# Optimization experiments

Measured on AMD Instinct MI355X. Metric: run time of the kernel, lower is better.

Reference implementation:

```python
import jax, jax.numpy as jnp
import numpy as np

N_NODES = 100000


def gcn_conv(x, W, b, src, dst, ew, n):
    """PyG GCNConv with edge_weight: add self-loops (weight 1), symmetric norm,
    linear transform, scatter-add aggregation, bias."""
    h = x @ W                                   # [N, F_out]
    # degree includes the self-loop weight of 1 per node
    deg = jnp.zeros((n,), dtype=x.dtype).at[dst].add(ew) + 1.0
    dinv = jax.lax.rsqrt(deg)                   # deg > 0 always (self-loop)
    norm = dinv[src] * ew * dinv[dst]           # [E]
    agg = jax.ops.segment_sum(h[src] * norm[:, None], dst, num_segments=n)
    # self-loop contribution: norm_ii = dinv[i]^2 * 1
    agg = agg + h * (dinv * dinv)[:, None]
    return agg + b


def setup_inputs() -> dict:
    key = jax.random.key(0)
    ks = jax.random.split(key, 9)
    N, E, F_in, F_h, F_out = N_NODES, 1600000, 128, 64, 10
    x = jax.random.normal(ks[0], (N, F_in), dtype=jnp.float32)
    edge_index = jax.random.randint(ks[1], (2, E), 0, N, dtype=jnp.int64)
    edge_weight = jax.random.uniform(ks[2], (E,), dtype=jnp.float32)
    def glorot(k, fi, fo):
        s = jnp.sqrt(6.0 / (fi + fo))
        return jax.random.uniform(k, (fi, fo), minval=-s, maxval=s, dtype=jnp.float32)
    return {
        "x": x,
        "edge_index": edge_index,
        "edge_weight": edge_weight,
        "W1": glorot(ks[3], F_in, F_h), "b1": jnp.zeros((F_h,), jnp.float32),
        "W2": glorot(ks[4], F_h, F_h), "b2": jnp.zeros((F_h,), jnp.float32),
        "Wfc": glorot(ks[5], F_h, F_out), "bfc": jnp.zeros((F_out,), jnp.float32),
    }


def reference(x, edge_index, edge_weight, W1, b1, W2, b2, Wfc, bfc):
    n = x.shape[0]
    src, dst = edge_index[0], edge_index[1]
    h = gcn_conv(x, W1, b1, src, dst, edge_weight, n)
    h = jax.nn.relu(h)
    h = gcn_conv(h, W2, b2, src, dst, edge_weight, n)
    h = jax.nn.relu(h)
    return h @ Wfc + bfc
```

## Files before the change

### kernel.cpp

```cpp
#include <hip/hip_runtime.h>

static constexpr int F_IN  = 128;
static constexpr int F_H   = 64;
static constexpr int F_OUT = 10;

static constexpr int NPB_SHIFT = 9;
static constexpr int NPB = 1 << NPB_SHIFT;
static constexpr int MAXC = 256;
static constexpr int EPB = 4096;

__device__ __forceinline__ unsigned short f2bf(float f) {
    unsigned u = __float_as_uint(f);
    return (unsigned short)((u + 0x7fff + ((u >> 16) & 1)) >> 16);
}
__device__ __forceinline__ float bf_lo(unsigned u) { return __uint_as_float(u << 16); }
__device__ __forceinline__ float bf_hi(unsigned u) { return __uint_as_float(u & 0xffff0000u); }

__device__ __forceinline__ int load_idx(const void* ein, bool f64, long i) {
    return f64 ? (int)((const long long*)ein)[i] : ((const int*)ein)[i];
}

__global__ __launch_bounds__(256) void k_detect_init(const unsigned long long* __restrict__ u,
                                                     int* __restrict__ flag,
                                                     int* __restrict__ gcur) {
    int tid = threadIdx.x;
    if (tid < MAXC) gcur[tid] = 0;
    if (tid < 64) {
        unsigned long long v = u[tid];
        int hz = ((v >> 32) == 0ull) ? 1 : 0;
        int all64 = __all(hz);
        if (tid == 0) flag[0] = all64;
    }
}

__global__ __launch_bounds__(256) void k_part1(const void* __restrict__ ein,
                                               const float* __restrict__ ew,
                                               const int* __restrict__ flag,
                                               int* __restrict__ gcur,
                                               unsigned long long* __restrict__ packed,
                                               int E, int NC, int cap) {
    __shared__ int lcnt[MAXC];
    __shared__ int lofs[MAXC];
    int tid = threadIdx.x;
    if (tid < NC) lcnt[tid] = 0;
    __syncthreads();
    bool f = flag[0];
    int base = blockIdx.x * EPB;
#pragma unroll
    for (int j = 0; j < EPB / 256; ++j) {
        int e = base + j * 256 + tid;
        if (e < E) {
            int d = load_idx(ein, f, (long)E + e);
            atomicAdd(&lcnt[d >> NPB_SHIFT], 1);
        }
    }
    __syncthreads();
    if (tid < NC) {
        int c = lcnt[tid];
        lofs[tid] = c ? atomicAdd(&gcur[tid], c) : 0;
        lcnt[tid] = 0;
    }
    __syncthreads();
#pragma unroll
    for (int j = 0; j < EPB / 256; ++j) {
        int e = base + j * 256 + tid;
        if (e < E) {
            int s = load_idx(ein, f, e);
            int d = load_idx(ein, f, (long)E + e);
            unsigned int wb = __float_as_uint(ew[e]);
            int b = d >> NPB_SHIFT;
            int pos = lofs[b] + atomicAdd(&lcnt[b], 1);
            if (pos < cap) {
                unsigned long long u = (unsigned long long)wb
                                     | ((unsigned long long)(unsigned)s << 32)
                                     | ((unsigned long long)(unsigned)(d & (NPB - 1)) << 49);
                packed[(long)b * cap + pos] = u;
            }
        }
    }
}

__global__ __launch_bounds__(256) void k_chist(const unsigned long long* __restrict__ packed,
                                               const int* __restrict__ gcur,
                                               int* __restrict__ rp,
                                               int* __restrict__ pbt,
                                               float* __restrict__ dinv,
                                               int N, int cap) {
    __shared__ int   lc[NPB];
    __shared__ float ld[NPB];
    __shared__ int   sm[256];
    int b = blockIdx.x, tid = threadIdx.x;
#pragma unroll
    for (int i = tid; i < NPB; i += 256) { lc[i] = 0; ld[i] = 0.0f; }
    __syncthreads();
    int cnt = gcur[b];
    const unsigned long long* pk = packed + (long)b * cap;
    for (int p = tid; p < cnt; p += 256) {
        unsigned long long u = pk[p];
        int dl = (int)(u >> 49);
        atomicAdd(&lc[dl], 1);
        atomicAdd(&ld[dl], __uint_as_float((unsigned int)u));
    }
    __syncthreads();
    int c0 = lc[tid * 2], c1 = lc[tid * 2 + 1];
    int pp0 = (c0 + 15) & ~15, pp1 = (c1 + 15) & ~15;
    int s = pp0 + pp1;
    sm[tid] = s;
    __syncthreads();
    for (int off = 1; off < 256; off <<= 1) {
        int v = 0;
        if (tid >= off) v = sm[tid - off];
        __syncthreads();
        sm[tid] += v;
        __syncthreads();
    }
    int excl = sm[tid] - s;
    int n0 = b << NPB_SHIFT;
    int node0 = n0 + tid * 2, node1 = node0 + 1;
    if (node0 < N) {
        rp[node0]   = excl;
        dinv[node0] = rsqrtf(ld[tid * 2] + 1.0f);
    }
    if (node1 < N) {
        rp[node1]   = excl + pp0;
        dinv[node1] = rsqrtf(ld[tid * 2 + 1] + 1.0f);
    }
    if (tid == 255) pbt[b] = sm[255];
}

__global__ __launch_bounds__(256) void k_scanP(const int* __restrict__ pbt,
                                               int* __restrict__ pbase,
                                               int* __restrict__ rp, int NC, int N) {
    __shared__ int sm[256];
    int tid = threadIdx.x;
    int c = (tid < NC) ? pbt[tid] : 0;
    sm[tid] = c;
    __syncthreads();
    for (int off = 1; off < 256; off <<= 1) {
        int v = 0;
        if (tid >= off) v = sm[tid - off];
        __syncthreads();
        sm[tid] += v;
        __syncthreads();
    }
    if (tid < NC) pbase[tid] = sm[tid] - c;
    if (tid == 255) rp[N] = sm[255];
}

__global__ __launch_bounds__(256) void k_rpfix(int* __restrict__ rp,
                                               const int* __restrict__ pbase, int N) {
    int i = blockIdx.x * 256 + threadIdx.x;
    if (i < N) rp[i] += pbase[i >> NPB_SHIFT];
}

__global__ __launch_bounds__(256) void k_cscatter(const unsigned long long* __restrict__ packed,
                                                  const int* __restrict__ gcur,
                                                  const int* __restrict__ rp,
                                                  const float* __restrict__ dinv,
                                                  uint2* __restrict__ recs,
                                                  int N, int cap) {
    __shared__ int   cur[NPB];
    __shared__ float dd[NPB];
    int b = blockIdx.x, tid = threadIdx.x;
    int n0 = b << NPB_SHIFT;
#pragma unroll
    for (int i = tid; i < NPB; i += 256) {
        int node = n0 + i;
        cur[i] = (node < N) ? rp[node]   : 0;
        dd[i]  = (node < N) ? dinv[node] : 0.0f;
    }
    __syncthreads();
    int cnt = gcur[b];
    const unsigned long long* pk = packed + (long)b * cap;
    for (int p = tid; p < cnt; p += 256) {
        unsigned long long u = pk[p];
        int dl = (int)(u >> 49);
        int s  = (int)((u >> 32) & 0x1FFFF);
        float w = __uint_as_float((unsigned int)u);
        int pos = atomicAdd(&cur[dl], 1);
        uint2 r;
        r.x = (unsigned)(s << 7);
        r.y = __float_as_uint(dinv[s] * w * dd[dl]);
        recs[pos] = r;
    }
    __syncthreads();
    for (int i = tid; i < NPB; i += 256) {
        int node = n0 + i;
        if (node < N) {
            int end = rp[node + 1];
            for (int p = cur[i]; p < end; ++p) recs[p] = make_uint2(0u, 0u);
        }
    }
}

template <int K>
__global__ __launch_bounds__(256) void k_gemm(const float* __restrict__ A,
                                              const float* __restrict__ W,
                                              unsigned short* __restrict__ Cb, int M) {
    __shared__ float As[128][32];
    __shared__ float Ws[32][64];
    int tid = threadIdx.x;
    int tx = tid & 15;
    int ty = tid >> 4;
    int rb = blockIdx.x * 128;
    float acc[8][4] = {};
    for (int kc = 0; kc < K; kc += 32) {
        __syncthreads();
#pragma unroll
        for (int i = 0; i < 4; ++i) {
            int e = tid + i * 256;
            int r = e >> 3, g = e & 7;
            int gr = rb + r;
            float4 v = make_float4(0.f, 0.f, 0.f, 0.f);
            if (gr < M) v = *(const float4*)&A[(long)gr * K + kc + g * 4];
            int gs = g ^ ((r >> 3) & 7);
            *(float4*)&As[r][gs * 4] = v;
        }
#pragma unroll
        for (int i = 0; i < 2; ++i) {
            int e = tid + i * 256;
            int k = e >> 4, n4 = e & 15;
            *(float4*)&Ws[k][n4 * 4] = *(const float4*)&W[(long)(kc + k) * 64 + n4 * 4];
        }
        __syncthreads();
#pragma unroll
        for (int g = 0; g < 8; ++g) {
            float4 b0 = *(const float4*)&Ws[g * 4 + 0][tx * 4];
            float4 b1 = *(const float4*)&Ws[g * 4 + 1][tx * 4];
            float4 b2 = *(const float4*)&Ws[g * 4 + 2][tx * 4];
            float4 b3 = *(const float4*)&Ws[g * 4 + 3][tx * 4];
            int gs = (g ^ (ty & 7)) * 4;
#pragma unroll
            for (int rr = 0; rr < 8; ++rr) {
                float4 a = *(const float4*)&As[ty * 8 + rr][gs];
                acc[rr][0] = fmaf(a.x, b0.x, acc[rr][0]);
                acc[rr][1] = fmaf(a.x, b0.y, acc[rr][1]);
                acc[rr][2] = fmaf(a.x, b0.z, acc[rr][2]);
                acc[rr][3] = fmaf(a.x, b0.w, acc[rr][3]);
                acc[rr][0] = fmaf(a.y, b1.x, acc[rr][0]);
                acc[rr][1] = fmaf(a.y, b1.y, acc[rr][1]);
                acc[rr][2] = fmaf(a.y, b1.z, acc[rr][2]);
                acc[rr][3] = fmaf(a.y, b1.w, acc[rr][3]);
                acc[rr][0] = fmaf(a.z, b2.x, acc[rr][0]);
                acc[rr][1] = fmaf(a.z, b2.y, acc[rr][1]);
                acc[rr][2] = fmaf(a.z, b2.z, acc[rr][2]);
                acc[rr][3] = fmaf(a.z, b2.w, acc[rr][3]);
                acc[rr][0] = fmaf(a.w, b3.x, acc[rr][0]);
                acc[rr][1] = fmaf(a.w, b3.y, acc[rr][1]);
                acc[rr][2] = fmaf(a.w, b3.z, acc[rr][2]);
                acc[rr][3] = fmaf(a.w, b3.w, acc[rr][3]);
            }
        }
    }
#pragma unroll
    for (int rr = 0; rr < 8; ++rr) {
        int gr = rb + ty * 8 + rr;
        if (gr < M) {
            ushort4 v;
            v.x = f2bf(acc[rr][0]); v.y = f2bf(acc[rr][1]);
            v.z = f2bf(acc[rr][2]); v.w = f2bf(acc[rr][3]);
            *(ushort4*)&Cb[(long)gr * 64 + tx * 4] = v;
        }
    }
}

__global__ __launch_bounds__(256, 4) void k_agg(const unsigned short* __restrict__ hb,
                                                const int* __restrict__ rp,
                                                const uint2* __restrict__ recs,
                                                const float* __restrict__ dinv,
                                                const float* __restrict__ bias,
                                                float* __restrict__ out, int N) {
    int wid  = (blockIdx.x * 256 + threadIdx.x) >> 6;
    int lane = threadIdx.x & 63;
    int fg   = lane & 15;
    int es   = lane >> 4;
    if (wid >= N) return;
    int fg8 = fg * 8;
    const char* hbase = (const char*)hb;
    int p0 = rp[wid], p1 = rp[wid + 1];
    float a0 = 0.f, a1 = 0.f, a2 = 0.f, a3 = 0.f;
    for (int pb = p0 + es * 4; pb < p1; pb += 16) {
        uint4 r01 = *(const uint4*)&recs[pb];
        uint4 r23 = *(const uint4*)&recs[pb + 2];
        uint2 h0 = *(const uint2*)(hbase + r01.x + fg8);
        uint2 h1 = *(const uint2*)(hbase + r01.z + fg8);
        uint2 h2 = *(const uint2*)(hbase + r23.x + fg8);
        uint2 h3 = *(const uint2*)(hbase + r23.z + fg8);
        float w0 = __uint_as_float(r01.y), w1 = __uint_as_float(r01.w);
        float w2 = __uint_as_float(r23.y), w3 = __uint_as_float(r23.w);
        a0 = fmaf(w0, bf_lo(h0.x), a0); a1 = fmaf(w0, bf_hi(h0.x), a1);
        a2 = fmaf(w0, bf_lo(h0.y), a2); a3 = fmaf(w0, bf_hi(h0.y), a3);
        a0 = fmaf(w1, bf_lo(h1.x), a0); a1 = fmaf(w1, bf_hi(h1.x), a1);
        a2 = fmaf(w1, bf_lo(h1.y), a2); a3 = fmaf(w1, bf_hi(h1.y), a3);
        a0 = fmaf(w2, bf_lo(h2.x), a0); a1 = fmaf(w2, bf_hi(h2.x), a1);
        a2 = fmaf(w2, bf_lo(h2.y), a2); a3 = fmaf(w2, bf_hi(h2.y), a3);
        a0 = fmaf(w3, bf_lo(h3.x), a0); a1 = fmaf(w3, bf_hi(h3.x), a1);
        a2 = fmaf(w3, bf_lo(h3.y), a2); a3 = fmaf(w3, bf_hi(h3.y), a3);
    }
#pragma unroll
    for (int m = 16; m <= 32; m <<= 1) {
        a0 += __shfl_xor(a0, m);
        a1 += __shfl_xor(a1, m);
        a2 += __shfl_xor(a2, m);
        a3 += __shfl_xor(a3, m);
    }
    float di  = dinv[wid];
    float di2 = di * di;
    uint2 hs = *(const uint2*)(hbase + ((long)wid << 7) + fg8);
    float4 bv = *(const float4*)&bias[fg * 4];
    a0 = fmaf(bf_lo(hs.x), di2, a0 + bv.x);
    a1 = fmaf(bf_hi(hs.x), di2, a1 + bv.y);
    a2 = fmaf(bf_lo(hs.y), di2, a2 + bv.z);
    a3 = fmaf(bf_hi(hs.y), di2, a3 + bv.w);
    if (es == 0) {
        float4 r = make_float4(fmaxf(a0, 0.f), fmaxf(a1, 0.f),
                               fmaxf(a2, 0.f), fmaxf(a3, 0.f));
        *(float4*)&out[(long)wid * 64 + fg * 4] = r;
    }
}

__global__ __launch_bounds__(256) void k_fc(const float* __restrict__ h,
                                            const float* __restrict__ W,
                                            const float* __restrict__ b,
                                            float* __restrict__ out, int N) {
    __shared__ float Ws[64 * 10];
    __shared__ float bs[16];
    int tid = threadIdx.x;
    for (int e = tid; e < 64 * 10; e += 256) Ws[e] = W[e];
    if (tid < 10) bs[tid] = b[tid];
    __syncthreads();
    int i = blockIdx.x * 256 + tid;
    if (i >= N) return;
    float acc[10];
#pragma unroll
    for (int j = 0; j < 10; ++j) acc[j] = bs[j];
    const float4* row = (const float4*)&h[(long)i * 64];
#pragma unroll
    for (int c = 0; c < 16; ++c) {
        float4 a = row[c];
#pragma unroll
        for (int j = 0; j < 10; ++j) {
            acc[j] = fmaf(a.x, Ws[(4 * c + 0) * 10 + j], acc[j]);
            acc[j] = fmaf(a.y, Ws[(4 * c + 1) * 10 + j], acc[j]);
            acc[j] = fmaf(a.z, Ws[(4 * c + 2) * 10 + j], acc[j]);
            acc[j] = fmaf(a.w, Ws[(4 * c + 3) * 10 + j], acc[j]);
        }
    }
#pragma unroll
    for (int j = 0; j < 10; ++j) out[(long)i * 10 + j] = acc[j];
}

extern "C" void kernel_launch(void* const* d_in, const int* in_sizes, int n_in,
                              void* d_out, int out_size, void* d_ws, size_t ws_size,
                              hipStream_t stream) {
    const float* x    = (const float*)d_in[0];
    const void*  eidx = d_in[1];
    const float* ew   = (const float*)d_in[2];
    const float* W1   = (const float*)d_in[3];
    const float* b1   = (const float*)d_in[4];
    const float* W2   = (const float*)d_in[5];
    const float* b2   = (const float*)d_in[6];
    const float* Wfc  = (const float*)d_in[7];
    const float* bfc  = (const float*)d_in[8];
    float* out = (float*)d_out;

    const int N  = in_sizes[0] / F_IN;
    const int E  = in_sizes[2];
    const int NC = (N + NPB - 1) >> NPB_SHIFT;
    const int cap = E / NC + E / (8 * NC) + 1024;

    char* w = (char*)d_ws;
    size_t off = 0;
    auto alloc = [&](size_t bytes) {
        void* p = w + off;
        off += (bytes + 255) & ~(size_t)255;
        return p;
    };
    float* dinv  = (float*)alloc((size_t)N * 4);
    int*   rp    = (int*)alloc((size_t)(N + 1) * 4);
    int*   flag  = (int*)alloc(256);
    int*   gcur  = (int*)alloc((size_t)MAXC * 4);
    int*   pbt   = (int*)alloc((size_t)MAXC * 4);
    int*   pbase = (int*)alloc((size_t)MAXC * 4);
    unsigned long long* packed =
        (unsigned long long*)alloc((size_t)NC * cap * 8);
    uint2* recs  = (uint2*)alloc(((size_t)E + 15u * (size_t)N + 64) * 8);
    unsigned short* h1b = (unsigned short*)alloc((size_t)N * F_H * 2);
    float* g1    = (float*)alloc((size_t)N * F_H * 4);
    unsigned short* h2b = h1b;
    float* g2    = g1;
    (void)ws_size;

    const int PB = (E + EPB - 1) / EPB;

    k_detect_init<<<1, 256, 0, stream>>>((const unsigned long long*)eidx, flag, gcur);
    k_part1<<<PB, 256, 0, stream>>>(eidx, ew, flag, gcur, packed, E, NC, cap);
    k_chist<<<NC, 256, 0, stream>>>(packed, gcur, rp, pbt, dinv, N, cap);
    k_scanP<<<1, 256, 0, stream>>>(pbt, pbase, rp, NC, N);
    k_rpfix<<<(N + 255) / 256, 256, 0, stream>>>(rp, pbase, N);
    k_cscatter<<<NC, 256, 0, stream>>>(packed, gcur, rp, dinv, recs, N, cap);

    const int GB = (N + 127) / 128;
    k_gemm<F_IN><<<GB, 256, 0, stream>>>(x, W1, h1b, N);
    k_agg<<<(N + 3) / 4, 256, 0, stream>>>(h1b, rp, recs, dinv, b1, g1, N);
    k_gemm<F_H><<<GB, 256, 0, stream>>>(g1, W2, h2b, N);
    k_agg<<<(N + 3) / 4, 256, 0, stream>>>(h2b, rp, recs, dinv, b2, g2, N);
    k_fc<<<(N + 255) / 256, 256, 0, stream>>>(g2, Wfc, bfc, out, N);
}
```

Measured before the change: 215.9 us.

## Store aggregation outputs as bf16 and fold rowptr fixup into scatter kernel

The aggregation kernels now write their ReLU'd outputs as bf16 instead of fp32, and the second GEMM and the final FC read bf16 inputs. This halves the bytes of the intermediate feature buffers. The k_detect_init and k_rpfix launches are removed: the index-width flag is computed per block inside k_part1, gcur is cleared with a memset, and absolute row pointers are built inside k_cscatter from the per-partition base. Rounding the layer outputs to bf16 adds some precision loss, and an extra rowptr array is written.

New measurement: 216.9 us. No clear change (+0.5%).

```diff
diff --git a/kernel.cpp b/kernel.cpp
--- a/kernel.cpp
+++ b/kernel.cpp
@@ -20,31 +20,24 @@
     return f64 ? (int)((const long long*)ein)[i] : ((const int*)ein)[i];
 }
 
-__global__ __launch_bounds__(256) void k_detect_init(const unsigned long long* __restrict__ u,
-                                                     int* __restrict__ flag,
-                                                     int* __restrict__ gcur) {
-    int tid = threadIdx.x;
-    if (tid < MAXC) gcur[tid] = 0;
-    if (tid < 64) {
-        unsigned long long v = u[tid];
-        int hz = ((v >> 32) == 0ull) ? 1 : 0;
-        int all64 = __all(hz);
-        if (tid == 0) flag[0] = all64;
-    }
-}
-
 __global__ __launch_bounds__(256) void k_part1(const void* __restrict__ ein,
                                                const float* __restrict__ ew,
-                                               const int* __restrict__ flag,
                                                int* __restrict__ gcur,
                                                unsigned long long* __restrict__ packed,
                                                int E, int NC, int cap) {
     __shared__ int lcnt[MAXC];
     __shared__ int lofs[MAXC];
+    __shared__ int sflag;
     int tid = threadIdx.x;
     if (tid < NC) lcnt[tid] = 0;
-    __syncthreads();
-    bool f = flag[0];
+    if (tid < 64) {
+        unsigned long long v = ((const unsigned long long*)ein)[tid];
+        int hz = ((v >> 32) == 0ull) ? 1 : 0;
+        int all64 = __all(hz);
+        if (tid == 0) sflag = all64;
+    }
+    __syncthreads();
+    bool f = sflag != 0;
     int base = blockIdx.x * EPB;
 #pragma unroll
     for (int j = 0; j < EPB / 256; ++j) {
@@ -130,7 +123,7 @@
 
 __global__ __launch_bounds__(256) void k_scanP(const int* __restrict__ pbt,
                                                int* __restrict__ pbase,
-                                               int* __restrict__ rp, int NC, int N) {
+                                               int* __restrict__ rpabs, int NC, int N) {
     __shared__ int sm[256];
     int tid = threadIdx.x;
     int c = (tid < NC) ? pbt[tid] : 0;
@@ -144,30 +137,30 @@
         __syncthreads();
     }
     if (tid < NC) pbase[tid] = sm[tid] - c;
-    if (tid == 255) rp[N] = sm[255];
-}
-
-__global__ __launch_bounds__(256) void k_rpfix(int* __restrict__ rp,
-                                               const int* __restrict__ pbase, int N) {
-    int i = blockIdx.x * 256 + threadIdx.x;
-    if (i < N) rp[i] += pbase[i >> NPB_SHIFT];
+    if (tid == 255) rpabs[N] = sm[255];
 }
 
 __global__ __launch_bounds__(256) void k_cscatter(const unsigned long long* __restrict__ packed,
                                                   const int* __restrict__ gcur,
                                                   const int* __restrict__ rp,
+                                                  const int* __restrict__ pbase,
+                                                  const int* __restrict__ pbt,
                                                   const float* __restrict__ dinv,
                                                   uint2* __restrict__ recs,
+                                                  int* __restrict__ rpabs,
                                                   int N, int cap) {
     __shared__ int   cur[NPB];
     __shared__ float dd[NPB];
     int b = blockIdx.x, tid = threadIdx.x;
     int n0 = b << NPB_SHIFT;
+    int pb_ = pbase[b];
 #pragma unroll
     for (int i = tid; i < NPB; i += 256) {
         int node = n0 + i;
-        cur[i] = (node < N) ? rp[node]   : 0;
+        int r = (node < N) ? rp[node] + pb_ : 0;
+        cur[i] = r;
         dd[i]  = (node < N) ? dinv[node] : 0.0f;
+        if (node < N) rpabs[node] = r;
     }
     __syncthreads();
     int cnt = gcur[b];
@@ -187,14 +180,15 @@
     for (int i = tid; i < NPB; i += 256) {
         int node = n0 + i;
         if (node < N) {
-            int end = rp[node + 1];
+            int el = (i == NPB - 1 || node + 1 >= N) ? pbt[b] : rp[node + 1];
+            int end = el + pb_;
             for (int p = cur[i]; p < end; ++p) recs[p] = make_uint2(0u, 0u);
         }
     }
 }
 
-template <int K>
-__global__ __launch_bounds__(256) void k_gemm(const float* __restrict__ A,
+template <int K, bool ABF16>
+__global__ __launch_bounds__(256) void k_gemm(const void* __restrict__ A,
                                               const float* __restrict__ W,
                                               unsigned short* __restrict__ Cb, int M) {
     __shared__ float As[128][32];
@@ -212,7 +206,14 @@
             int r = e >> 3, g = e & 7;
             int gr = rb + r;
             float4 v = make_float4(0.f, 0.f, 0.f, 0.f);
-            if (gr < M) v = *(const float4*)&A[(long)gr * K + kc + g * 4];
+            if (gr < M) {
+                if (ABF16) {
+                    uint2 u = *(const uint2*)&((const unsigned short*)A)[(long)gr * K + kc + g * 4];
+                    v = make_float4(bf_lo(u.x), bf_hi(u.x), bf_lo(u.y), bf_hi(u.y));
+                } else {
+                    v = *(const float4*)&((const float*)A)[(long)gr * K + kc + g * 4];
+                }
+            }
             int gs = g ^ ((r >> 3) & 7);
             *(float4*)&As[r][gs * 4] = v;
         }
@@ -269,7 +270,7 @@
                                                 const uint2* __restrict__ recs,
                                                 const float* __restrict__ dinv,
                                                 const float* __restrict__ bias,
-                                                float* __restrict__ out, int N) {
+                                                unsigned short* __restrict__ outb, int N) {
     int wid  = (blockIdx.x * 256 + threadIdx.x) >> 6;
     int lane = threadIdx.x & 63;
     int fg   = lane & 15;
@@ -313,13 +314,16 @@
     a2 = fmaf(bf_lo(hs.y), di2, a2 + bv.z);
     a3 = fmaf(bf_hi(hs.y), di2, a3 + bv.w);
     if (es == 0) {
-        float4 r = make_float4(fmaxf(a0, 0.f), fmaxf(a1, 0.f),
-                               fmaxf(a2, 0.f), fmaxf(a3, 0.f));
-        *(float4*)&out[(long)wid * 64 + fg * 4] = r;
-    }
-}
-
-__global__ __launch_bounds__(256) void k_fc(const float* __restrict__ h,
+        ushort4 r;
+        r.x = f2bf(fmaxf(a0, 0.f));
+        r.y = f2bf(fmaxf(a1, 0.f));
+        r.z = f2bf(fmaxf(a2, 0.f));
+        r.w = f2bf(fmaxf(a3, 0.f));
+        *(ushort4*)&outb[(long)wid * 64 + fg * 4] = r;
+    }
+}
+
+__global__ __launch_bounds__(256) void k_fc(const unsigned short* __restrict__ hb,
                                             const float* __restrict__ W,
                                             const float* __restrict__ b,
                                             float* __restrict__ out, int N) {
@@ -334,16 +338,18 @@
     float acc[10];
 #pragma unroll
     for (int j = 0; j < 10; ++j) acc[j] = bs[j];
-    const float4* row = (const float4*)&h[(long)i * 64];
+    const uint2* row = (const uint2*)&hb[(long)i * 64];
 #pragma unroll
     for (int c = 0; c < 16; ++c) {
-        float4 a = row[c];
+        uint2 u = row[c];
+        float ax = bf_lo(u.x), ay = bf_hi(u.x);
+        float az = bf_lo(u.y), aw = bf_hi(u.y);
 #pragma unroll
         for (int j = 0; j < 10; ++j) {
-            acc[j] = fmaf(a.x, Ws[(4 * c + 0) * 10 + j], acc[j]);
-            acc[j] = fmaf(a.y, Ws[(4 * c + 1) * 10 + j], acc[j]);
-            acc[j] = fmaf(a.z, Ws[(4 * c + 2) * 10 + j], acc[j]);
-            acc[j] = fmaf(a.w, Ws[(4 * c + 3) * 10 + j], acc[j]);
+            acc[j] = fmaf(ax, Ws[(4 * c + 0) * 10 + j], acc[j]);
+            acc[j] = fmaf(ay, Ws[(4 * c + 1) * 10 + j], acc[j]);
+            acc[j] = fmaf(az, Ws[(4 * c + 2) * 10 + j], acc[j]);
+            acc[j] = fmaf(aw, Ws[(4 * c + 3) * 10 + j], acc[j]);
         }
     }
 #pragma unroll
@@ -378,7 +384,7 @@
     };
     float* dinv  = (float*)alloc((size_t)N * 4);
     int*   rp    = (int*)alloc((size_t)(N + 1) * 4);
-    int*   flag  = (int*)alloc(256);
+    int*   rpabs = (int*)alloc((size_t)(N + 1) * 4);
     int*   gcur  = (int*)alloc((size_t)MAXC * 4);
     int*   pbt   = (int*)alloc((size_t)MAXC * 4);
     int*   pbase = (int*)alloc((size_t)MAXC * 4);
@@ -386,24 +392,25 @@
         (unsigned long long*)alloc((size_t)NC * cap * 8);
     uint2* recs  = (uint2*)alloc(((size_t)E + 15u * (size_t)N + 64) * 8);
     unsigned short* h1b = (unsigned short*)alloc((size_t)N * F_H * 2);
-    float* g1    = (float*)alloc((size_t)N * F_H * 4);
+    unsigned short* g1b = (unsigned short*)alloc((size_t)N * F_H * 2);
     unsigned short* h2b = h1b;
-    float* g2    = g1;
+    unsigned short* g2b = g1b;
     (void)ws_size;
 
+    hipMemsetAsync(gcur, 0, (size_t)NC * 4, stream);
+
     const int PB = (E + EPB - 1) / EPB;
 
-    k_detect_init<<<1, 256, 0, stream>>>((const unsigned long long*)eidx, flag, gcur);
-    k_part1<<<PB, 256, 0, stream>>>(eidx, ew, flag, gcur, packed, E, NC, cap);
+    k_part1<<<PB, 256, 0, stream>>>(eidx, ew, gcur, packed, E, NC, cap);
     k_chist<<<NC, 256, 0, stream>>>(packed, gcur, rp, pbt, dinv, N, cap);
-    k_scanP<<<1, 256, 0, stream>>>(pbt, pbase, rp, NC, N);
-    k_rpfix<<<(N + 255) / 256, 256, 0, stream>>>(rp, pbase, N);
-    k_cscatter<<<NC, 256, 0, stream>>>(packed, gcur, rp, dinv, recs, N, cap);
+    k_scanP<<<1, 256, 0, stream>>>(pbt, pbase, rpabs, NC, N);
+    k_cscatter<<<NC, 256, 0, stream>>>(packed, gcur, rp, pbase, pbt, dinv, recs,
+                                       rpabs, N, cap);
 
     const int GB = (N + 127) / 128;
-    k_gemm<F_IN><<<GB, 256, 0, stream>>>(x, W1, h1b, N);
-    k_agg<<<(N + 3) / 4, 256, 0, stream>>>(h1b, rp, recs, dinv, b1, g1, N);
-    k_gemm<F_H><<<GB, 256, 0, stream>>>(g1, W2, h2b, N);
-    k_agg<<<(N + 3) / 4, 256, 0, stream>>>(h2b, rp, recs, dinv, b2, g2, N);
-    k_fc<<<(N + 255) / 256, 256, 0, stream>>>(g2, Wfc, bfc, out, N);
-}
+    k_gemm<F_IN, false><<<GB, 256, 0, stream>>>(x, W1, h1b, N);
+    k_agg<<<(N + 3) / 4, 256, 0, stream>>>(h1b, rpabs, recs, dinv, b1, g1b, N);
+    k_gemm<F_H, true><<<GB, 256, 0, stream>>>(g1b, W2, h2b, N);
+    k_agg<<<(N + 3) / 4, 256, 0, stream>>>(h2b, rpabs, recs, dinv, b2, g2b, N);
+    k_fc<<<(N + 255) / 256, 256, 0, stream>>>(g2b, Wfc, bfc, out, N);
+}
```
